# Kernel optimization log

Measured on AMD Instinct MI355X. Metric: run time of the kernel, lower is better.

## Reference

```python
import jax, jax.numpy as jnp
import numpy as np

B, V, D, H, ET = 32, 50, 6, 256, 4  # batch, num_vars, input_size, decoder_hidden, num_edge_types
E = V * (V - 1)                      # fully connected, no self-loops


def setup_inputs() -> dict:
    key = jax.random.key(0)
    ks = jax.random.split(key, 24)
    s = 0.05
    n = lambda k, shape: jax.random.normal(k, shape, jnp.float32)
    return {
        "inputs": n(ks[0], (B, V, D)),
        "hidden": n(ks[1], (B, V, H)),
        "edges": jax.random.uniform(ks[2], (B, E, ET), jnp.float32),
        # stacked per-edge-type message MLPs for the non-skipped types 1..ET-1
        "W1": n(ks[3], (ET - 1, H, 2 * H)) * s, "b1": jnp.full((ET - 1, H), 0.1, jnp.float32),
        "W2": n(ks[4], (ET - 1, H, H)) * s, "b2": jnp.full((ET - 1, H), 0.1, jnp.float32),
        # GRU-style update (hidden_* have no bias in the torch module)
        "Whr": n(ks[5], (H, H)) * s, "Whi": n(ks[6], (H, H)) * s, "Whh": n(ks[7], (H, H)) * s,
        "Wir": n(ks[8], (H, D)) * s, "bir": jnp.full((H,), 0.1, jnp.float32),
        "Wii": n(ks[9], (H, D)) * s, "bii": jnp.full((H,), 0.1, jnp.float32),
        "Win": n(ks[10], (H, D)) * s, "bin_w": jnp.full((H,), 0.1, jnp.float32),
        # output MLP
        "Wo1": n(ks[11], (H, H)) * s, "bo1": jnp.full((H,), 0.1, jnp.float32),
        "Wo2": n(ks[12], (H, H)) * s, "bo2": jnp.full((H,), 0.1, jnp.float32),
        "Wo3": n(ks[13], (D, H)) * s, "bo3": jnp.full((D,), 0.1, jnp.float32),
    }


def _edge_index(num_vars):
    mask = np.ones((num_vars, num_vars)) - np.eye(num_vars)
    send, recv = np.where(mask)
    onehot = np.zeros((send.shape[0], num_vars), dtype=np.float32)
    onehot[np.arange(send.shape[0]), recv] = 1.0  # edge2node scatter matrix [E, V]
    return send, recv, onehot


def reference(inputs, hidden, edges, W1, b1, W2, b2, Whr, Whi, Whh,
              Wir, bir, Wii, bii, Win, bin_w, Wo1, bo1, Wo2, bo2, Wo3, bo3):
    num_vars = hidden.shape[1]
    send, recv, onehot = _edge_index(num_vars)
    onehot = jnp.asarray(onehot)

    # gather: [B, E, 2H]
    pre_msg = jnp.concatenate([hidden[:, recv, :], hidden[:, send, :]], axis=-1)

    # per-edge-type message MLP (dropout is identity in eval mode), types 1..ET-1 (skip_first)
    m = jnp.tanh(jnp.einsum('bef,thf->bteh', pre_msg, W1) + b1[None, :, None, :])
    m = jnp.tanh(jnp.einsum('bteh,tgh->bteg', m, W2) + b2[None, :, None, :])
    ew = jnp.moveaxis(edges[:, :, 1:], -1, 1)          # [B, T, E]
    norm = edges.shape[-1] - 1
    all_msgs = jnp.einsum('bteh,bte->beh', m, ew) / norm  # [B, E, H]

    # scatter-aggregate edges -> receiver nodes
    agg = jnp.einsum('beh,ev->bvh', all_msgs, onehot) / (num_vars - 1)  # [B, V, H]

    # GRU-style gated update
    r = jax.nn.sigmoid(inputs @ Wir.T + bir + agg @ Whr.T)
    i = jax.nn.sigmoid(inputs @ Wii.T + bii + agg @ Whi.T)
    n_ = jnp.tanh(inputs @ Win.T + bin_w + r * (agg @ Whh.T))
    hidden_new = (1 - i) * n_ + i * hidden

    # output MLP with residual on inputs
    p = jax.nn.relu(hidden_new @ Wo1.T + bo1)
    p = jax.nn.relu(p @ Wo2.T + bo2)
    pred = inputs + (p @ Wo3.T + bo3)
    return pred, hidden_new
```

## Files before the change

kernel.cpp:

```cpp
#include <hip/hip_runtime.h>
#include <math.h>

#define B_ 32
#define V_ 50
#define D_ 6
#define H_ 256
#define E_ 2450
#define T_ 3
#define NN 1600

#define OFF_inputs 0
#define OFF_hidden 9600
#define OFF_edges  419200
#define OFF_W1     732800
#define OFF_b1     1126016
#define OFF_W2     1126784
#define OFF_b2     1323392
#define OFF_Whr    1324160
#define OFF_Whi    1389696
#define OFF_Whh    1455232
#define OFF_Wir    1520768
#define OFF_bir    1522304
#define OFF_Wii    1522560
#define OFF_bii    1524096
#define OFF_Win    1524352
#define OFF_binw   1525888
#define OFF_Wo1    1526144
#define OFF_bo1    1591680
#define OFF_Wo2    1591936
#define OFF_bo2    1657472
#define OFF_Wo3    1657728
#define OFF_bo3    1659264
#define TOTAL_IN   1659270

#define PW_W2   0
#define PW_W1   196608
#define PW_WG   589824
#define PW_WO1  786432
#define PW_WO2  851968
#define PW_HID  917504
#define PW_TOT  1327104

typedef __attribute__((ext_vector_type(8))) short short8;
typedef __attribute__((ext_vector_type(4))) float f32x4;

__device__ __forceinline__ float bfc(unsigned int u) {
    return __uint_as_float((u & 0xffffu) << 16);
}
__device__ __forceinline__ unsigned short f2bf(float f) {
    unsigned int x = __float_as_uint(f);
    unsigned int r = (x + 0x7fffu + ((x >> 16) & 1u)) >> 16;
    return (unsigned short)r;
}
__device__ __forceinline__ float tanh_fast(float x) {
    float e = __builtin_amdgcn_exp2f(x * 2.8853900817779268f);
    return 1.0f - 2.0f * __builtin_amdgcn_rcpf(1.0f + e);
}
__device__ __forceinline__ float sigmoid_fast(float x) {
    float e = __builtin_amdgcn_exp2f(x * -1.4426950408889634f);
    return __builtin_amdgcn_rcpf(1.0f + e);
}

struct Ptrs { const void* p[22]; };

__device__ __forceinline__ int detect_bf(const Ptrs& pt) {
    const unsigned short* b1r = (const unsigned short*)pt.p[4];
    return (b1r[0] == 0x3DCDu && b1r[1] == 0x3DCDu) ? 1 : 0;
}
__device__ __forceinline__ float ldraw(const Ptrs& pt, int bf, int ti, int li) {
    return bf ? bfc(((const unsigned short*)pt.p[ti])[li])
              : ((const float*)pt.p[ti])[li];
}

__global__ __launch_bounds__(256) void kprepA(Ptrs pt, float* __restrict__ stag,
                                              unsigned short* __restrict__ W2s,
                                              unsigned short* __restrict__ W1s,
                                              unsigned short* __restrict__ Wgs,
                                              unsigned short* __restrict__ Wo1s,
                                              unsigned short* __restrict__ Wo2s,
                                              unsigned short* __restrict__ hidbf) {
    int i = blockIdx.x * 256 + threadIdx.x;
    if (i >= TOTAL_IN + PW_TOT) return;
    int bf = detect_bf(pt);
    if (i < TOTAL_IN) {
        int ti, base;
        if      (i < OFF_hidden) { ti = 0;  base = OFF_inputs; }
        else if (i < OFF_edges)  { ti = 1;  base = OFF_hidden; }
        else if (i < OFF_W1)     { ti = 2;  base = OFF_edges;  }
        else if (i < OFF_b1)     { ti = 3;  base = OFF_W1;     }
        else if (i < OFF_W2)     { ti = 4;  base = OFF_b1;     }
        else if (i < OFF_b2)     { ti = 5;  base = OFF_W2;     }
        else if (i < OFF_Whr)    { ti = 6;  base = OFF_b2;     }
        else if (i < OFF_Whi)    { ti = 7;  base = OFF_Whr;    }
        else if (i < OFF_Whh)    { ti = 8;  base = OFF_Whi;    }
        else if (i < OFF_Wir)    { ti = 9;  base = OFF_Whh;    }
        else if (i < OFF_bir)    { ti = 10; base = OFF_Wir;    }
        else if (i < OFF_Wii)    { ti = 11; base = OFF_bir;    }
        else if (i < OFF_bii)    { ti = 12; base = OFF_Wii;    }
        else if (i < OFF_Win)    { ti = 13; base = OFF_bii;    }
        else if (i < OFF_binw)   { ti = 14; base = OFF_Win;    }
        else if (i < OFF_Wo1)    { ti = 15; base = OFF_binw;   }
        else if (i < OFF_bo1)    { ti = 16; base = OFF_Wo1;    }
        else if (i < OFF_Wo2)    { ti = 17; base = OFF_bo1;    }
        else if (i < OFF_bo2)    { ti = 18; base = OFF_Wo2;    }
        else if (i < OFF_Wo3)    { ti = 19; base = OFF_bo2;    }
        else if (i < OFF_bo3)    { ti = 20; base = OFF_Wo3;    }
        else                     { ti = 21; base = OFF_bo3;    }
        stag[i] = ldraw(pt, bf, ti, i - base);
        return;
    }
    int ii = i - TOTAL_IN;
    if (ii < PW_W1) {
        int j = ii & 7, l = (ii >> 3) & 63;
        int rest = ii >> 9;
        int ntg = rest & 15, k0 = (rest >> 4) & 7, t = rest >> 7;
        int g = ntg * 16 + (l & 15);
        int k = k0 * 32 + ((l >> 4) << 3) + j;
        W2s[ii] = f2bf(ldraw(pt, bf, 5, (t * H_ + g) * H_ + k));
    } else if (ii < PW_WG) {
        int i1 = ii - PW_W1;
        int j = i1 & 7, l = (i1 >> 3) & 63;
        int rest = i1 >> 9;
        int ntg = rest % 96, k0 = rest / 96;
        int n = ntg * 16 + (l & 15);
        int t = n >> 9, half = (n >> 8) & 1, h = n & 255;
        int k = k0 * 32 + ((l >> 4) << 3) + j;
        W1s[i1] = f2bf(ldraw(pt, bf, 3, (t * H_ + h) * (2 * H_) + half * H_ + k));
    } else if (ii < PW_WO1) {
        int i2 = ii - PW_WG;
        int j = i2 & 7, l = (i2 >> 3) & 63;
        int rest = i2 >> 9;
        int ntg = rest % 48, k0 = rest / 48;
        int n = ntg * 16 + (l & 15);
        int gate = n >> 8, h = n & 255;
        int k = k0 * 32 + ((l >> 4) << 3) + j;
        Wgs[i2] = f2bf(ldraw(pt, bf, 7 + gate, h * H_ + k));
    } else if (ii < PW_WO2) {
        int i3 = ii - PW_WO1;
        int j = i3 & 7, l = (i3 >> 3) & 63;
        int rest = i3 >> 9;
        int ntg = rest & 15, k0 = rest >> 4;
        int h = ntg * 16 + (l & 15);
        int k = k0 * 32 + ((l >> 4) << 3) + j;
        Wo1s[i3] = f2bf(ldraw(pt, bf, 16, h * H_ + k));
    } else if (ii < PW_HID) {
        int i4 = ii - PW_WO2;
        int j = i4 & 7, l = (i4 >> 3) & 63;
        int rest = i4 >> 9;
        int ntg = rest & 15, k0 = rest >> 4;
        int h = ntg * 16 + (l & 15);
        int k = k0 * 32 + ((l >> 4) << 3) + j;
        Wo2s[i4] = f2bf(ldraw(pt, bf, 18, h * H_ + k));
    } else {
        int i5 = ii - PW_HID;
        hidbf[i5] = f2bf(ldraw(pt, bf, 1, i5));
    }
}

__global__ __launch_bounds__(256) void k1M(const unsigned short* __restrict__ hidbf,
                                           const unsigned short* __restrict__ W1s,
                                           float* __restrict__ Hr, float* __restrict__ Hs) {
    int m0 = blockIdx.x * 64;
    int nb = blockIdx.y;
    int t = nb >> 1, half = nb & 1;
    int tid = threadIdx.x;
    int w = tid >> 6, l = tid & 63, l15 = l & 15, quad = l >> 4;

    f32x4 acc[4][4];
    #pragma unroll
    for (int mt = 0; mt < 4; mt++)
        #pragma unroll
        for (int nt = 0; nt < 4; nt++) acc[mt][nt] = (f32x4){0.f, 0.f, 0.f, 0.f};

    for (int k0 = 0; k0 < 8; k0++) {
        short8 af[4], bfr[4];
        #pragma unroll
        for (int mt = 0; mt < 4; mt++) {
            int node = m0 + mt * 16 + l15;
            af[mt] = *(const short8*)&hidbf[node * H_ + k0 * 32 + quad * 8];
        }
        #pragma unroll
        for (int nt = 0; nt < 4; nt++) {
            int ntg = nb * 16 + w * 4 + nt;
            bfr[nt] = *(const short8*)&W1s[((k0 * 96 + ntg) << 9) + (l << 3)];
        }
        #pragma unroll
        for (int mt = 0; mt < 4; mt++)
            #pragma unroll
            for (int nt = 0; nt < 4; nt++)
                acc[mt][nt] = __builtin_amdgcn_mfma_f32_16x16x32_bf16(
                    af[mt], bfr[nt], acc[mt][nt], 0, 0, 0);
    }

    float* dst = half ? Hs : Hr;
    #pragma unroll
    for (int mt = 0; mt < 4; mt++)
        #pragma unroll
        for (int nt = 0; nt < 4; nt++) {
            int h = w * 64 + nt * 16 + l15;
            #pragma unroll
            for (int r = 0; r < 4; r++) {
                int node = m0 + mt * 16 + quad * 4 + r;
                dst[((size_t)t * NN + node) * H_ + h] = acc[mt][nt][r];
            }
        }
}

__global__ __launch_bounds__(256, 4) void k2(const float* __restrict__ stag,
                                          const float* __restrict__ Hr, const float* __restrict__ Hs,
                                          const unsigned short* __restrict__ W2s,
                                          unsigned short* __restrict__ aggbf) {
    int bv = blockIdx.x;
    int b = bv / V_;
    int v = bv % V_;
    int tid = threadIdx.x;
    int w = tid >> 6, l = tid & 63, l15 = l & 15, quad = l >> 4;

    __shared__ __align__(16) unsigned short m1A[32 * 64 * 8];
    __shared__ float hrb3[T_][H_];
    __shared__ float sew[T_][64];
    __shared__ int ssend[64];

    if (tid < 64) {
        int j = tid;
        int s = (j < 49) ? (j + (j >= v ? 1 : 0)) : v;
        ssend[j] = s;
        if (j < 49) {
            int e = s * (V_ - 1) + (v > s ? v - 1 : v);
            #pragma unroll
            for (int t = 0; t < T_; t++)
                sew[t][j] = stag[OFF_edges + ((size_t)b * E_ + e) * 4 + 1 + t];
        } else {
            #pragma unroll
            for (int t = 0; t < T_; t++) sew[t][j] = 0.f;
        }
    }
    #pragma unroll
    for (int t = 0; t < T_; t++)
        hrb3[t][tid] = Hr[(((size_t)t * B_ + b) * V_ + v) * H_ + tid]
                     + stag[OFF_b1 + t * H_ + tid];
    __syncthreads();

    float msgp[4] = {0.f, 0.f, 0.f, 0.f};
    int er = (w << 4) + l15;
    int snd = ssend[er];

    for (int t = 0; t < T_; t++) {
        const float* hsrow = Hs + (((size_t)t * B_ + b) * V_ + snd) * H_;
        #pragma unroll
        for (int i = 0; i < 8; i++) {
            int c = (quad + (i << 2)) << 3;
            float4 x0 = *(const float4*)(hsrow + c);
            float4 x1 = *(const float4*)(hsrow + c + 4);
            float4 h0 = *(const float4*)&hrb3[t][c];
            float4 h1 = *(const float4*)&hrb3[t][c + 4];
            unsigned short pk[8];
            pk[0] = f2bf(tanh_fast(x0.x + h0.x));
            pk[1] = f2bf(tanh_fast(x0.y + h0.y));
            pk[2] = f2bf(tanh_fast(x0.z + h0.z));
            pk[3] = f2bf(tanh_fast(x0.w + h0.w));
            pk[4] = f2bf(tanh_fast(x1.x + h1.x));
            pk[5] = f2bf(tanh_fast(x1.y + h1.y));
            pk[6] = f2bf(tanh_fast(x1.z + h1.z));
            pk[7] = f2bf(tanh_fast(x1.w + h1.w));
            *(short8*)&m1A[(((w << 3) + i) << 9) + (l << 3)] = *(short8*)pk;
        }
        __syncthreads();

        f32x4 acc[4][4];
        #pragma unroll
        for (int mt = 0; mt < 4; mt++)
            #pragma unroll
            for (int nt = 0; nt < 4; nt++) acc[mt][nt] = (f32x4){0.f, 0.f, 0.f, 0.f};

        for (int k0 = 0; k0 < 8; k0++) {
            short8 af[4], bfr[4];
            #pragma unroll
            for (int mt = 0; mt < 4; mt++)
                af[mt] = *(const short8*)&m1A[(((mt << 3) + k0) << 9) + (l << 3)];
            #pragma unroll
            for (int nt = 0; nt < 4; nt++) {
                int ntg = w * 4 + nt;
                bfr[nt] = *(const short8*)&W2s[((((t * 8 + k0) * 16 + ntg) << 6) + l) << 3];
            }
            #pragma unroll
            for (int mt = 0; mt < 4; mt++)
                #pragma unroll
                for (int nt = 0; nt < 4; nt++)
                    acc[mt][nt] = __builtin_amdgcn_mfma_f32_16x16x32_bf16(
                        af[mt], bfr[nt], acc[mt][nt], 0, 0, 0);
        }

        #pragma unroll
        for (int nt = 0; nt < 4; nt++) {
            float b2v = stag[OFF_b2 + t * H_ + w * 64 + nt * 16 + l15];
            float p = 0.f;
            #pragma unroll
            for (int mt = 0; mt < 4; mt++) {
                #pragma unroll
                for (int r = 0; r < 4; r++) {
                    int row = mt * 16 + quad * 4 + r;
                    p += sew[t][row] * tanh_fast(acc[mt][nt][r] + b2v);
                }
            }
            msgp[nt] += p;
        }
        __syncthreads();
    }

    const float scale = 1.0f / ((float)T_ * (float)(V_ - 1));
    #pragma unroll
    for (int nt = 0; nt < 4; nt++) {
        float vs = msgp[nt];
        vs += __shfl_xor(vs, 16, 64);
        vs += __shfl_xor(vs, 32, 64);
        if (quad == 0)
            aggbf[(size_t)bv * H_ + w * 64 + nt * 16 + l15] = f2bf(vs * scale);
    }
}

__global__ __launch_bounds__(256) void k4f(Ptrs pt, const float* __restrict__ stag,
                                           const unsigned short* __restrict__ aggbf,
                                           const unsigned short* __restrict__ Wgs,
                                           const unsigned short* __restrict__ Wo1s,
                                           const unsigned short* __restrict__ Wo2s,
                                           void* __restrict__ dout) {
    int n0 = blockIdx.x * 16;
    int tid = threadIdx.x;
    int w = tid >> 6, l = tid & 63, l15 = l & 15, quad = l >> 4;
    int bf = detect_bf(pt);

    __shared__ __align__(16) unsigned short bufA[16][264];
    __shared__ __align__(16) unsigned short bufB[16][264];

    f32x4 acc[3][4];
    #pragma unroll
    for (int g = 0; g < 3; g++)
        #pragma unroll
        for (int nt = 0; nt < 4; nt++) acc[g][nt] = (f32x4){0.f, 0.f, 0.f, 0.f};

    for (int k0 = 0; k0 < 8; k0++) {
        short8 af = *(const short8*)&aggbf[(n0 + l15) * H_ + k0 * 32 + quad * 8];
        #pragma unroll
        for (int g = 0; g < 3; g++)
            #pragma unroll
            for (int nt = 0; nt < 4; nt++) {
                int ntg = g * 16 + w * 4 + nt;
                short8 bfr = *(const short8*)&Wgs[((k0 * 48 + ntg) << 9) + (l << 3)];
                acc[g][nt] = __builtin_amdgcn_mfma_f32_16x16x32_bf16(
                    af, bfr, acc[g][nt], 0, 0, 0);
            }
    }

    float inp[4][D_];
    #pragma unroll
    for (int r = 0; r < 4; r++) {
        int node = n0 + quad * 4 + r;
        #pragma unroll
        for (int d = 0; d < D_; d++) inp[r][d] = stag[OFF_inputs + node * D_ + d];
    }
    #pragma unroll
    for (int nt = 0; nt < 4; nt++) {
        int h = w * 64 + nt * 16 + l15;
        float wir[D_], wii[D_], win[D_];
        #pragma unroll
        for (int d = 0; d < D_; d++) {
            wir[d] = stag[OFF_Wir + h * D_ + d];
            wii[d] = stag[OFF_Wii + h * D_ + d];
            win[d] = stag[OFF_Win + h * D_ + d];
        }
        float br = stag[OFF_bir + h], bi = stag[OFF_bii + h], bn = stag[OFF_binw + h];
        #pragma unroll
        for (int r = 0; r < 4; r++) {
            int node = n0 + quad * 4 + r;
            float xr = br, xi = bi, xn = bn;
            #pragma unroll
            for (int d = 0; d < D_; d++) {
                xr += inp[r][d] * wir[d];
                xi += inp[r][d] * wii[d];
                xn += inp[r][d] * win[d];
            }
            float rg = sigmoid_fast(xr + acc[0][nt][r]);
            float ig = sigmoid_fast(xi + acc[1][nt][r]);
            float ng = tanh_fast(xn + rg * acc[2][nt][r]);
            float hprev = stag[OFF_hidden + (size_t)node * H_ + h];
            float hn = (1.f - ig) * ng + ig * hprev;
            unsigned short hb = f2bf(hn);
            bufA[quad * 4 + r][h] = hb;
            if (bf) ((unsigned short*)dout)[9600 + (size_t)node * H_ + h] = hb;
            else    ((float*)dout)[9600 + (size_t)node * H_ + h] = hn;
        }
    }
    __syncthreads();

    {
        f32x4 a1[4];
        #pragma unroll
        for (int nt = 0; nt < 4; nt++) a1[nt] = (f32x4){0.f, 0.f, 0.f, 0.f};
        for (int k0 = 0; k0 < 8; k0++) {
            short8 af = *(const short8*)&bufA[l15][k0 * 32 + quad * 8];
            #pragma unroll
            for (int nt = 0; nt < 4; nt++) {
                int ntg = w * 4 + nt;
                short8 bfr = *(const short8*)&Wo1s[((k0 * 16 + ntg) << 9) + (l << 3)];
                a1[nt] = __builtin_amdgcn_mfma_f32_16x16x32_bf16(af, bfr, a1[nt], 0, 0, 0);
            }
        }
        __syncthreads();
        #pragma unroll
        for (int nt = 0; nt < 4; nt++) {
            int h = w * 64 + nt * 16 + l15;
            float bo = stag[OFF_bo1 + h];
            #pragma unroll
            for (int r = 0; r < 4; r++)
                bufB[quad * 4 + r][h] = f2bf(fmaxf(a1[nt][r] + bo, 0.f));
        }
    }
    __syncthreads();

    {
        f32x4 a2[4];
        #pragma unroll
        for (int nt = 0; nt < 4; nt++) a2[nt] = (f32x4){0.f, 0.f, 0.f, 0.f};
        for (int k0 = 0; k0 < 8; k0++) {
            short8 af = *(const short8*)&bufB[l15][k0 * 32 + quad * 8];
            #pragma unroll
            for (int nt = 0; nt < 4; nt++) {
                int ntg = w * 4 + nt;
                short8 bfr = *(const short8*)&Wo2s[((k0 * 16 + ntg) << 9) + (l << 3)];
                a2[nt] = __builtin_amdgcn_mfma_f32_16x16x32_bf16(af, bfr, a2[nt], 0, 0, 0);
            }
        }
        __syncthreads();
        #pragma unroll
        for (int nt = 0; nt < 4; nt++) {
            int h = w * 64 + nt * 16 + l15;
            float bo = stag[OFF_bo2 + h];
            #pragma unroll
            for (int r = 0; r < 4; r++)
                bufA[quad * 4 + r][h] = f2bf(fmaxf(a2[nt][r] + bo, 0.f));
        }
    }
    __syncthreads();

    if (tid < 16 * D_) {
        int nl = tid / D_, d = tid % D_;
        const float* wrow = stag + OFF_Wo3 + d * H_;
        float a = stag[OFF_bo3 + d];
        for (int k = 0; k < H_; k += 8) {
            short8 pv = *(const short8*)&bufA[nl][k];
            float4 w0 = *(const float4*)(wrow + k);
            float4 w1 = *(const float4*)(wrow + k + 4);
            a += bfc((unsigned short)pv[0]) * w0.x + bfc((unsigned short)pv[1]) * w0.y
               + bfc((unsigned short)pv[2]) * w0.z + bfc((unsigned short)pv[3]) * w0.w
               + bfc((unsigned short)pv[4]) * w1.x + bfc((unsigned short)pv[5]) * w1.y
               + bfc((unsigned short)pv[6]) * w1.z + bfc((unsigned short)pv[7]) * w1.w;
        }
        int node = n0 + nl;
        float val = a + stag[OFF_inputs + node * D_ + d];
        if (bf) ((unsigned short*)dout)[node * D_ + d] = f2bf(val);
        else    ((float*)dout)[node * D_ + d] = val;
    }
}

extern "C" void kernel_launch(void* const* d_in, const int* in_sizes, int n_in,
                              void* d_out, int out_size, void* d_ws, size_t ws_size,
                              hipStream_t stream) {
    float* stag = (float*)d_ws;
    float* Hr   = stag + 1659272;
    float* Hs   = Hr + 1228800;
    unsigned short* aggbf = (unsigned short*)(Hs + 1228800);
    unsigned short* W2s   = (unsigned short*)((float*)aggbf + 204800);
    unsigned short* W1s   = (unsigned short*)((float*)W2s + 98304);
    unsigned short* Wgs   = (unsigned short*)((float*)W1s + 196608);
    unsigned short* Wo1s  = (unsigned short*)((float*)Wgs + 98304);
    unsigned short* Wo2s  = (unsigned short*)((float*)Wo1s + 32768);
    unsigned short* hidbf = (unsigned short*)((float*)Wo2s + 32768);

    Ptrs pt;
    for (int i = 0; i < 22; i++) pt.p[i] = d_in[i];

    kprepA<<<(TOTAL_IN + PW_TOT + 255) / 256, 256, 0, stream>>>(pt, stag, W2s, W1s, Wgs, Wo1s, Wo2s, hidbf);
    k1M<<<dim3(25, 6), 256, 0, stream>>>(hidbf, W1s, Hr, Hs);
    k2<<<B_ * V_, 256, 0, stream>>>(stag, Hr, Hs, W2s, aggbf);
    k4f<<<NN / 16, 256, 0, stream>>>(pt, stag, aggbf, Wgs, Wo1s, Wo2s, d_out);
}
```

Baseline: 206.7 us.

## Pack edges densely into 64-row chunks in k2 with atomic receiver aggregation

Restructures the message kernel to tile the 2450 edges per batch densely into 64-row chunks instead of one padded 49-of-64 tile per receiver node, removing wasted MFMA and tanh work on padding rows. Each chunk splits partial sums across up to three receiver nodes and combines them via float atomicAdd into a zeroed fp32 aggregate buffer. The b1 bias is folded into the first GEMM's epilogue, and the consumer converts the fp32 aggregate to bf16 on load. This adds atomics, extra zeroing and non-deterministic summation order.

```diff
diff --git a/kernel.cpp b/kernel.cpp
--- a/kernel.cpp
+++ b/kernel.cpp
@@ -1,4 +1,5 @@
 #include <hip/hip_runtime.h>
+#include <hip/hip_bf16.h>
 #include <math.h>
 
 #define B_ 32
@@ -8,6 +9,7 @@
 #define E_ 2450
 #define T_ 3
 #define NN 1600
+#define CHUNKS 39
 
 #define OFF_inputs 0
 #define OFF_hidden 9600
@@ -40,6 +42,7 @@
 #define PW_WO2  851968
 #define PW_HID  917504
 #define PW_TOT  1327104
+#define AGG_N   409600
 
 typedef __attribute__((ext_vector_type(8))) short short8;
 typedef __attribute__((ext_vector_type(4))) float f32x4;
@@ -48,9 +51,7 @@
     return __uint_as_float((u & 0xffffu) << 16);
 }
 __device__ __forceinline__ unsigned short f2bf(float f) {
-    unsigned int x = __float_as_uint(f);
-    unsigned int r = (x + 0x7fffu + ((x >> 16) & 1u)) >> 16;
-    return (unsigned short)r;
+    return __builtin_bit_cast(unsigned short, __float2bfloat16(f));
 }
 __device__ __forceinline__ float tanh_fast(float x) {
     float e = __builtin_amdgcn_exp2f(x * 2.8853900817779268f);
@@ -78,9 +79,10 @@
                                               unsigned short* __restrict__ Wgs,
                                               unsigned short* __restrict__ Wo1s,
                                               unsigned short* __restrict__ Wo2s,
-                                              unsigned short* __restrict__ hidbf) {
+                                              unsigned short* __restrict__ hidbf,
+                                              float* __restrict__ aggf) {
     int i = blockIdx.x * 256 + threadIdx.x;
-    if (i >= TOTAL_IN + PW_TOT) return;
+    if (i >= TOTAL_IN + PW_TOT + AGG_N) return;
     int bf = detect_bf(pt);
     if (i < TOTAL_IN) {
         int ti, base;
@@ -151,14 +153,17 @@
         int h = ntg * 16 + (l & 15);
         int k = k0 * 32 + ((l >> 4) << 3) + j;
         Wo2s[i4] = f2bf(ldraw(pt, bf, 18, h * H_ + k));
-    } else {
+    } else if (ii < PW_TOT) {
         int i5 = ii - PW_HID;
         hidbf[i5] = f2bf(ldraw(pt, bf, 1, i5));
+    } else {
+        aggf[ii - PW_TOT] = 0.f;
     }
 }
 
 __global__ __launch_bounds__(256) void k1M(const unsigned short* __restrict__ hidbf,
                                            const unsigned short* __restrict__ W1s,
+                                           const float* __restrict__ stag,
                                            float* __restrict__ Hr, float* __restrict__ Hs) {
     int m0 = blockIdx.x * 64;
     int nb = blockIdx.y;
@@ -198,62 +203,68 @@
         #pragma unroll
         for (int nt = 0; nt < 4; nt++) {
             int h = w * 64 + nt * 16 + l15;
+            float bias = half ? 0.f : stag[OFF_b1 + t * H_ + h];
             #pragma unroll
             for (int r = 0; r < 4; r++) {
                 int node = m0 + mt * 16 + quad * 4 + r;
-                dst[((size_t)t * NN + node) * H_ + h] = acc[mt][nt][r];
-            }
-        }
-}
-
-__global__ __launch_bounds__(256, 4) void k2(const float* __restrict__ stag,
-                                          const float* __restrict__ Hr, const float* __restrict__ Hs,
-                                          const unsigned short* __restrict__ W2s,
-                                          unsigned short* __restrict__ aggbf) {
-    int bv = blockIdx.x;
-    int b = bv / V_;
-    int v = bv % V_;
+                dst[((size_t)t * NN + node) * H_ + h] = acc[mt][nt][r] + bias;
+            }
+        }
+}
+
+__global__ __launch_bounds__(512, 6) void k2(const float* __restrict__ stag,
+                                             const float* __restrict__ Hr,
+                                             const float* __restrict__ Hs,
+                                             const unsigned short* __restrict__ W2s,
+                                             float* __restrict__ aggf) {
+    int c = blockIdx.x, b = blockIdx.y;
+    int m0 = c * 64;
     int tid = threadIdx.x;
     int w = tid >> 6, l = tid & 63, l15 = l & 15, quad = l >> 4;
+    int mtW = w >> 1, half4 = (w & 1) * 4;
 
     __shared__ __align__(16) unsigned short m1A[32 * 64 * 8];
-    __shared__ float hrb3[T_][H_];
     __shared__ float sew[T_][64];
-    __shared__ int ssend[64];
 
     if (tid < 64) {
-        int j = tid;
-        int s = (j < 49) ? (j + (j >= v ? 1 : 0)) : v;
-        ssend[j] = s;
-        if (j < 49) {
-            int e = s * (V_ - 1) + (v > s ? v - 1 : v);
+        int mR = m0 + tid;
+        if (mR < E_) {
+            int vv = mR / 49, j = mR - vv * 49;
+            int ss = j + (j >= vv ? 1 : 0);
+            int e = ss * (V_ - 1) + (vv > ss ? vv - 1 : vv);
             #pragma unroll
             for (int t = 0; t < T_; t++)
-                sew[t][j] = stag[OFF_edges + ((size_t)b * E_ + e) * 4 + 1 + t];
+                sew[t][tid] = stag[OFF_edges + ((size_t)b * E_ + e) * 4 + 1 + t];
         } else {
             #pragma unroll
-            for (int t = 0; t < T_; t++) sew[t][j] = 0.f;
-        }
-    }
-    #pragma unroll
-    for (int t = 0; t < T_; t++)
-        hrb3[t][tid] = Hr[(((size_t)t * B_ + b) * V_ + v) * H_ + tid]
-                     + stag[OFF_b1 + t * H_ + tid];
-    __syncthreads();
-
-    float msgp[4] = {0.f, 0.f, 0.f, 0.f};
-    int er = (w << 4) + l15;
-    int snd = ssend[er];
+            for (int t = 0; t < T_; t++) sew[t][tid] = 0.f;
+        }
+    }
+
+    int rowT = mtW * 16 + l15;
+    int mT_ = m0 + rowT;
+    int vThr = 0, sThr = 0;
+    if (mT_ < E_) {
+        vThr = mT_ / 49; int j = mT_ - vThr * 49;
+        sThr = j + (j >= vThr ? 1 : 0);
+    }
+
+    int v0 = m0 / 49;
+    int B1 = (v0 + 1) * 49, B2 = B1 + 49;
+
+    float tot0 = 0.f, tot1 = 0.f, hi0 = 0.f, hi1 = 0.f, hh0 = 0.f, hh1 = 0.f;
 
     for (int t = 0; t < T_; t++) {
-        const float* hsrow = Hs + (((size_t)t * B_ + b) * V_ + snd) * H_;
-        #pragma unroll
-        for (int i = 0; i < 8; i++) {
-            int c = (quad + (i << 2)) << 3;
-            float4 x0 = *(const float4*)(hsrow + c);
-            float4 x1 = *(const float4*)(hsrow + c + 4);
-            float4 h0 = *(const float4*)&hrb3[t][c];
-            float4 h1 = *(const float4*)&hrb3[t][c + 4];
+        const float* hsrow = Hs + (((size_t)t * B_ + b) * V_ + sThr) * H_;
+        const float* hrrow = Hr + (((size_t)t * B_ + b) * V_ + vThr) * H_;
+        #pragma unroll
+        for (int i = 0; i < 4; i++) {
+            int k0 = half4 + i;
+            int cc = k0 * 32 + quad * 8;
+            float4 x0 = *(const float4*)(hsrow + cc);
+            float4 h0 = *(const float4*)(hrrow + cc);
+            float4 x1 = *(const float4*)(hsrow + cc + 4);
+            float4 h1 = *(const float4*)(hrrow + cc + 4);
             unsigned short pk[8];
             pk[0] = f2bf(tanh_fast(x0.x + h0.x));
             pk[1] = f2bf(tanh_fast(x0.y + h0.y));
@@ -263,64 +274,83 @@
             pk[5] = f2bf(tanh_fast(x1.y + h1.y));
             pk[6] = f2bf(tanh_fast(x1.z + h1.z));
             pk[7] = f2bf(tanh_fast(x1.w + h1.w));
-            *(short8*)&m1A[(((w << 3) + i) << 9) + (l << 3)] = *(short8*)pk;
+            *(short8*)&m1A[(((mtW << 3) + k0) << 9) + (l << 3)] = *(short8*)pk;
         }
         __syncthreads();
 
-        f32x4 acc[4][4];
-        #pragma unroll
-        for (int mt = 0; mt < 4; mt++)
-            #pragma unroll
-            for (int nt = 0; nt < 4; nt++) acc[mt][nt] = (f32x4){0.f, 0.f, 0.f, 0.f};
-
+        f32x4 acc[4][2];
+        #pragma unroll
+        for (int mt = 0; mt < 4; mt++) {
+            acc[mt][0] = (f32x4){0.f, 0.f, 0.f, 0.f};
+            acc[mt][1] = (f32x4){0.f, 0.f, 0.f, 0.f};
+        }
+        __builtin_amdgcn_s_setprio(1);
         for (int k0 = 0; k0 < 8; k0++) {
-            short8 af[4], bfr[4];
-            #pragma unroll
-            for (int mt = 0; mt < 4; mt++)
-                af[mt] = *(const short8*)&m1A[(((mt << 3) + k0) << 9) + (l << 3)];
-            #pragma unroll
-            for (int nt = 0; nt < 4; nt++) {
-                int ntg = w * 4 + nt;
-                bfr[nt] = *(const short8*)&W2s[((((t * 8 + k0) * 16 + ntg) << 6) + l) << 3];
-            }
-            #pragma unroll
-            for (int mt = 0; mt < 4; mt++)
-                #pragma unroll
-                for (int nt = 0; nt < 4; nt++)
-                    acc[mt][nt] = __builtin_amdgcn_mfma_f32_16x16x32_bf16(
-                        af[mt], bfr[nt], acc[mt][nt], 0, 0, 0);
-        }
-
-        #pragma unroll
-        for (int nt = 0; nt < 4; nt++) {
-            float b2v = stag[OFF_b2 + t * H_ + w * 64 + nt * 16 + l15];
-            float p = 0.f;
+            int ntg0 = w * 2;
+            short8 bf0 = *(const short8*)&W2s[((((t * 8 + k0) * 16 + ntg0) << 6) + l) << 3];
+            short8 bf1 = *(const short8*)&W2s[((((t * 8 + k0) * 16 + ntg0 + 1) << 6) + l) << 3];
             #pragma unroll
             for (int mt = 0; mt < 4; mt++) {
-                #pragma unroll
-                for (int r = 0; r < 4; r++) {
-                    int row = mt * 16 + quad * 4 + r;
-                    p += sew[t][row] * tanh_fast(acc[mt][nt][r] + b2v);
-                }
-            }
-            msgp[nt] += p;
+                short8 af = *(const short8*)&m1A[(((mt << 3) + k0) << 9) + (l << 3)];
+                acc[mt][0] = __builtin_amdgcn_mfma_f32_16x16x32_bf16(af, bf0, acc[mt][0], 0, 0, 0);
+                acc[mt][1] = __builtin_amdgcn_mfma_f32_16x16x32_bf16(af, bf1, acc[mt][1], 0, 0, 0);
+            }
+        }
+        __builtin_amdgcn_s_setprio(0);
+
+        float b2v0 = stag[OFF_b2 + t * H_ + (w * 2) * 16 + l15];
+        float b2v1 = stag[OFF_b2 + t * H_ + (w * 2 + 1) * 16 + l15];
+        #pragma unroll
+        for (int mt = 0; mt < 4; mt++) {
+            #pragma unroll
+            for (int r = 0; r < 4; r++) {
+                int row = mt * 16 + quad * 4 + r;
+                int m = m0 + row;
+                float ewv = sew[t][row];
+                float c0 = ewv * tanh_fast(acc[mt][0][r] + b2v0);
+                float c1 = ewv * tanh_fast(acc[mt][1][r] + b2v1);
+                tot0 += c0; tot1 += c1;
+                hi0 += (m >= B1) ? c0 : 0.f;
+                hi1 += (m >= B1) ? c1 : 0.f;
+                hh0 += (m >= B2) ? c0 : 0.f;
+                hh1 += (m >= B2) ? c1 : 0.f;
+            }
         }
         __syncthreads();
     }
 
-    const float scale = 1.0f / ((float)T_ * (float)(V_ - 1));
-    #pragma unroll
-    for (int nt = 0; nt < 4; nt++) {
-        float vs = msgp[nt];
-        vs += __shfl_xor(vs, 16, 64);
-        vs += __shfl_xor(vs, 32, 64);
-        if (quad == 0)
-            aggbf[(size_t)bv * H_ + w * 64 + nt * 16 + l15] = f2bf(vs * scale);
+    float s00 = tot0 - hi0, s01 = tot1 - hi1;
+    float s10 = hi0 - hh0,  s11 = hi1 - hh1;
+    s00 += __shfl_xor(s00, 16, 64); s00 += __shfl_xor(s00, 32, 64);
+    s01 += __shfl_xor(s01, 16, 64); s01 += __shfl_xor(s01, 32, 64);
+    s10 += __shfl_xor(s10, 16, 64); s10 += __shfl_xor(s10, 32, 64);
+    s11 += __shfl_xor(s11, 16, 64); s11 += __shfl_xor(s11, 32, 64);
+    hh0 += __shfl_xor(hh0, 16, 64); hh0 += __shfl_xor(hh0, 32, 64);
+    hh1 += __shfl_xor(hh1, 16, 64); hh1 += __shfl_xor(hh1, 32, 64);
+
+    if (quad == 0) {
+        const float scale = 1.0f / ((float)T_ * (float)(V_ - 1));
+        int col0 = (w * 2) * 16 + l15;
+        size_t base0 = ((size_t)b * V_ + v0) * H_;
+        atomicAdd(&aggf[base0 + col0], s00 * scale);
+        atomicAdd(&aggf[base0 + col0 + 16], s01 * scale);
+        if (B1 < m0 + 64) {
+            int v1c = min(v0 + 1, V_ - 1);
+            size_t base1 = ((size_t)b * V_ + v1c) * H_;
+            atomicAdd(&aggf[base1 + col0], s10 * scale);
+            atomicAdd(&aggf[base1 + col0 + 16], s11 * scale);
+        }
+        if (B2 < m0 + 64) {
+            int v2c = min(v0 + 2, V_ - 1);
+            size_t base2 = ((size_t)b * V_ + v2c) * H_;
+            atomicAdd(&aggf[base2 + col0], hh0 * scale);
+            atomicAdd(&aggf[base2 + col0 + 16], hh1 * scale);
+        }
     }
 }
 
 __global__ __launch_bounds__(256) void k4f(Ptrs pt, const float* __restrict__ stag,
-                                           const unsigned short* __restrict__ aggbf,
+                                           const float* __restrict__ aggf,
                                            const unsigned short* __restrict__ Wgs,
                                            const unsigned short* __restrict__ Wo1s,
                                            const unsigned short* __restrict__ Wo2s,
@@ -340,7 +370,13 @@
         for (int nt = 0; nt < 4; nt++) acc[g][nt] = (f32x4){0.f, 0.f, 0.f, 0.f};
 
     for (int k0 = 0; k0 < 8; k0++) {
-        short8 af = *(const short8*)&aggbf[(n0 + l15) * H_ + k0 * 32 + quad * 8];
+        const float* ar = aggf + (size_t)(n0 + l15) * H_ + k0 * 32 + quad * 8;
+        float4 q0 = *(const float4*)ar;
+        float4 q1 = *(const float4*)(ar + 4);
+        unsigned short pk[8];
+        pk[0] = f2bf(q0.x); pk[1] = f2bf(q0.y); pk[2] = f2bf(q0.z); pk[3] = f2bf(q0.w);
+        pk[4] = f2bf(q1.x); pk[5] = f2bf(q1.y); pk[6] = f2bf(q1.z); pk[7] = f2bf(q1.w);
+        short8 af = *(const short8*)pk;
         #pragma unroll
         for (int g = 0; g < 3; g++)
             #pragma unroll
@@ -469,8 +505,8 @@
     float* stag = (float*)d_ws;
     float* Hr   = stag + 1659272;
     float* Hs   = Hr + 1228800;
-    unsigned short* aggbf = (unsigned short*)(Hs + 1228800);
-    unsigned short* W2s   = (unsigned short*)((float*)aggbf + 204800);
+    float* aggf = Hs + 1228800;
+    unsigned short* W2s   = (unsigned short*)(aggf + 409600);
     unsigned short* W1s   = (unsigned short*)((float*)W2s + 98304);
     unsigned short* Wgs   = (unsigned short*)((float*)W1s + 196608);
     unsigned short* Wo1s  = (unsigned short*)((float*)Wgs + 98304);
@@ -480,8 +516,9 @@
     Ptrs pt;
     for (int i = 0; i < 22; i++) pt.p[i] = d_in[i];
 
-    kprepA<<<(TOTAL_IN + PW_TOT + 255) / 256, 256, 0, stream>>>(pt, stag, W2s, W1s, Wgs, Wo1s, Wo2s, hidbf);
-    k1M<<<dim3(25, 6), 256, 0, stream>>>(hidbf, W1s, Hr, Hs);
-    k2<<<B_ * V_, 256, 0, stream>>>(stag, Hr, Hs, W2s, aggbf);
-    k4f<<<NN / 16, 256, 0, stream>>>(pt, stag, aggbf, Wgs, Wo1s, Wo2s, d_out);
-}
+    kprepA<<<(TOTAL_IN + PW_TOT + AGG_N + 255) / 256, 256, 0, stream>>>(
+        pt, stag, W2s, W1s, Wgs, Wo1s, Wo2s, hidbf, aggf);
+    k1M<<<dim3(25, 6), 256, 0, stream>>>(hidbf, W1s, stag, Hr, Hs);
+    k2<<<dim3(CHUNKS, B_), 512, 0, stream>>>(stag, Hr, Hs, W2s, aggf);
+    k4f<<<NN / 16, 256, 0, stream>>>(pt, stag, aggf, Wgs, Wo1s, Wo2s, d_out);
+}
```

New measurement: 228.1 us. 1.1x slower.
